# Performance work log

Hardware: AMD Instinct MI355X
Metric: run time of the kernel (lower is better)

Reference implementation:

```python
import jax, jax.numpy as jnp
import numpy as np

S = 2048        # q_len == context_length
HID = 4096      # hidden_size
NH = 32         # num_attention_heads
NKV = 8         # num_key_value_heads
HD = HID // NH  # head_dim = 128
THETA = 10000.0


def setup_inputs() -> dict:
    key = jax.random.key(0)
    ks = jax.random.split(key, 5)
    hidden_states = jax.random.normal(ks[0], (1, S, HID), dtype=jnp.float32)
    # 1x1 Conv2d weights == linear weights (out_ch, in_ch)
    wq = jax.random.normal(ks[1], (NH * HD, HID), dtype=jnp.float32) * 0.02
    wk = jax.random.normal(ks[2], (NKV * HD, HID), dtype=jnp.float32) * 0.02
    wv = jax.random.normal(ks[3], (NKV * HD, HID), dtype=jnp.float32) * 0.02
    wo = jax.random.normal(ks[4], (HID, NH * HD), dtype=jnp.float32) * 0.02
    # RoPE tables: rotate() only ever uses the first half_dim of cos/sin,
    # so build (1,1,S,half) directly (equivalent to cat(freqs,freqs) then slice).
    half = HD // 2
    inv_freq = 1.0 / (THETA ** (jnp.arange(0, HD, 2, dtype=jnp.float32) / HD))
    freqs = jnp.outer(jnp.arange(S, dtype=jnp.float32), inv_freq)  # (S, half)
    cos = jnp.cos(freqs)[None, None]  # (1,1,S,half)
    sin = jnp.sin(freqs)[None, None]
    # additive causal mask (1,1,S,S): 0 on/below diagonal, large negative above
    causal_mask = jnp.where(
        jnp.arange(S)[:, None] >= jnp.arange(S)[None, :], 0.0, -1e9
    ).astype(jnp.float32)[None, None]
    return dict(hidden_states=hidden_states, wq=wq, wk=wk, wv=wv, wo=wo,
                cos=cos, sin=sin, causal_mask=causal_mask)


def _rope(x, cos, sin):
    # x: (H, S, D); cos/sin: (1,1,S,D/2)
    half = x.shape[-1] // 2
    x1, x2 = x[..., :half], x[..., half:]
    c, s = cos[0, 0], sin[0, 0]  # (S, half), broadcasts over heads
    return jnp.concatenate([x1 * c - x2 * s, x2 * c + x1 * s], axis=-1)


def reference(hidden_states, wq, wk, wv, wo, cos, sin, causal_mask):
    x = hidden_states[0]               # (S, HID); bsz hard-coded to 1 in source
    seq = x.shape[0]
    # 1x1 conv projections == matmul; channel layout is head-major (h*HD + d)
    q = (x @ wq.T).reshape(seq, NH, HD).transpose(1, 0, 2)    # (NH, S, D)
    k = (x @ wk.T).reshape(seq, NKV, HD).transpose(1, 0, 2)   # (NKV, S, D)
    v = (x @ wv.T).reshape(seq, NKV, HD).transpose(1, 0, 2)   # (NKV, S, D)
    q = _rope(q, cos, sin)
    k = _rope(k, cos, sin)
    # repeat_kv: unsqueeze(1).repeat(n_rep).view -> head idx = rep*NKV + kv == tile
    n_rep = NH // NKV
    k = jnp.tile(k, (n_rep, 1, 1))     # (NH, S, D)
    v = jnp.tile(v, (n_rep, 1, 1))
    scale = 1.0 / np.sqrt(HD).astype(np.float32)
    scores = jnp.einsum('hqd,hkd->hqk', q, k) * scale + causal_mask[0, 0]
    attn = jax.nn.softmax(scores, axis=-1)                    # == ANE_softmax
    out = jnp.einsum('hqk,hkd->hqd', attn, v)                 # (NH, S, D)
    out = out.transpose(1, 0, 2).reshape(seq, NH * HD)        # (S, HID)
    return (out @ wo.T)[None]                                 # (1, S, HID)
```

## Files before the change

kernel.cpp:

```cpp
#include <hip/hip_runtime.h>
#include <hip/hip_bf16.h>

#define S_LEN 2048
#define HID   4096
#define NH    32
#define NKV   8
#define HD    128
#define QKV_N 6144
#define KDIM  4096

typedef __attribute__((ext_vector_type(8))) short short8;
typedef __attribute__((ext_vector_type(4))) float floatx4;
typedef unsigned short ushort;

__device__ __forceinline__ unsigned short f2bu(float f) {
  __hip_bfloat16 b = __float2bfloat16(f);
  return *reinterpret_cast<unsigned short*>(&b);
}
__device__ __forceinline__ void store_c(float* p, float v) { *p = v; }
__device__ __forceinline__ void store_c(__hip_bfloat16* p, float v) { *p = __float2bfloat16(v); }

__device__ __forceinline__ void async_copy16(const void* g, void* l) {
  __builtin_amdgcn_global_load_lds((const __attribute__((address_space(1))) void*)g,
                                   (__attribute__((address_space(3))) void*)l, 16, 0, 0);
}

struct bf16x4 { __hip_bfloat16 a, b, c, d; };
__global__ void cvt_f32_bf16(const float* __restrict__ src, __hip_bfloat16* __restrict__ dst, int n4) {
  int i = blockIdx.x * blockDim.x + threadIdx.x;
  if (i < n4) {
    float4 v = ((const float4*)src)[i];
    bf16x4 o = { __float2bfloat16(v.x), __float2bfloat16(v.y),
                 __float2bfloat16(v.z), __float2bfloat16(v.w) };
    ((bf16x4*)dst)[i] = o;
  }
}

template <typename CT>
__global__ __launch_bounds__(256, 2) void gemm_nt(const __hip_bfloat16* __restrict__ A,
                                                  const __hip_bfloat16* __restrict__ B,
                                                  CT* __restrict__ C, int M, int N, int K) {
  __shared__ __align__(16) ushort As[128 * 64];
  __shared__ __align__(16) ushort Bs[128 * 64];
  const int tid  = threadIdx.x;
  const int bm   = blockIdx.y * 128;
  const int bn   = blockIdx.x * 128;
  const int wave = tid >> 6;
  const int lane = tid & 63;
  const int ww   = (wave >> 1) * 64;
  const int wc   = (wave & 1) * 64;
  const int l15  = lane & 15;
  const int quad = lane >> 4;

  const ushort* Au = (const ushort*)A;
  const ushort* Bu = (const ushort*)B;

  const int rr  = lane >> 3;
  const int cc  = lane & 7;
  const int gch = cc ^ rr;
  const ushort* Ag = Au + (size_t)(bm + wave * 32 + rr) * K + gch * 8;
  const ushort* Bg = Bu + (size_t)(bn + wave * 32 + rr) * K + gch * 8;

  floatx4 acc[4][4] = {};

  for (int k0 = 0; k0 < K; k0 += 64) {
    __syncthreads();
#pragma unroll
    for (int e = 0; e < 4; ++e) {
      async_copy16(Ag + (size_t)(e * 8) * K + k0, &As[(wave * 32 + e * 8) * 64]);
      async_copy16(Bg + (size_t)(e * 8) * K + k0, &Bs[(wave * 32 + e * 8) * 64]);
    }
    __syncthreads();
#pragma unroll
    for (int kd = 0; kd < 2; ++kd) {
      short8 af[4], bf[4];
#pragma unroll
      for (int i = 0; i < 4; ++i) {
        af[i] = *(const short8*)&As[(ww + i * 16 + l15) * 64 + ((kd * 4 + quad) ^ (l15 & 7)) * 8];
        bf[i] = *(const short8*)&Bs[(wc + i * 16 + l15) * 64 + ((kd * 4 + quad) ^ (l15 & 7)) * 8];
      }
#pragma unroll
      for (int mi = 0; mi < 4; ++mi)
#pragma unroll
        for (int ni = 0; ni < 4; ++ni)
          acc[mi][ni] = __builtin_amdgcn_mfma_f32_16x16x32_bf16(af[mi], bf[ni], acc[mi][ni], 0, 0, 0);
    }
  }
#pragma unroll
  for (int mi = 0; mi < 4; ++mi)
#pragma unroll
    for (int ni = 0; ni < 4; ++ni)
#pragma unroll
      for (int r = 0; r < 4; ++r) {
        int row = bm + ww + mi * 16 + quad * 4 + r;
        int col = bn + wc + ni * 16 + l15;
        store_c(&C[(size_t)row * N + col], acc[mi][ni][r]);
      }
}

__global__ void rope_qk(const __hip_bfloat16* __restrict__ QKV,
                        const float* __restrict__ cosp, const float* __restrict__ sinp,
                        __hip_bfloat16* __restrict__ Qh, __hip_bfloat16* __restrict__ Kh) {
  int s = blockIdx.y;
  int col = blockIdx.x * 256 + threadIdx.x;
  if (col >= 5120) return;
  const size_t base = (size_t)s * QKV_N;
  float x = __bfloat162float(QKV[base + col]);
  int dd = col & 127;
  float val;
  if (dd < 64) {
    float xp = __bfloat162float(QKV[base + col + 64]);
    val = x * cosp[s * 64 + dd] - xp * sinp[s * 64 + dd];
  } else {
    int f = dd - 64;
    float xp = __bfloat162float(QKV[base + col - 64]);
    val = x * cosp[s * 64 + f] + xp * sinp[s * 64 + f];
  }
  if (col < HID) {
    int h = col >> 7;
    Qh[((size_t)h * S_LEN + s) * HD + dd] = __float2bfloat16(val);
  } else {
    int h = (col - HID) >> 7;
    Kh[((size_t)h * S_LEN + s) * HD + dd] = __float2bfloat16(val);
  }
}

__global__ void v_transpose(const __hip_bfloat16* __restrict__ QKV, __hip_bfloat16* __restrict__ Vt) {
  __shared__ ushort tile[64][130];
  int h = blockIdx.y;
  int s0 = blockIdx.x * 64;
  int t = threadIdx.x;
  const ushort* src = (const ushort*)QKV;
#pragma unroll
  for (int i = 0; i < 32; ++i) {
    int flat = i * 256 + t;
    int r = flat >> 7, c = flat & 127;
    tile[r][c] = src[(size_t)(s0 + r) * QKV_N + 5120 + h * 128 + c];
  }
  __syncthreads();
  ushort* dst = (ushort*)Vt;
#pragma unroll
  for (int i = 0; i < 8; ++i) {
    int g = i * 256 + t;
    int d = g >> 4, j4 = (g & 15) * 4;
    ushort4 o;
    o.x = tile[j4][d]; o.y = tile[j4 + 1][d]; o.z = tile[j4 + 2][d]; o.w = tile[j4 + 3][d];
    *(ushort4*)&dst[((size_t)h * HD + d) * S_LEN + s0 + j4] = o;
  }
}

__global__ __launch_bounds__(256, 2) void attn(const __hip_bfloat16* __restrict__ Qh,
                                               const __hip_bfloat16* __restrict__ Kh,
                                               const __hip_bfloat16* __restrict__ Vt,
                                               __hip_bfloat16* __restrict__ AO) {
  __shared__ __align__(16) ushort Ks[2][64][128];
  __shared__ __align__(16) ushort P[4][32][72];
  const int bi   = blockIdx.x;
  const int head = bi & 31;
  const int slot = (bi >> 5) & 7;
  const int qt   = (bi >= 256) ? (2 * slot) : (15 - 2 * slot);
  const int wave = threadIdx.x >> 6;
  const int lane = threadIdx.x & 63;
  const int l15 = lane & 15, quad = lane >> 4;
  const int q0 = qt * 128 + wave * 32;
  const int hk = head & 7;
  const ushort* Qu = (const ushort*)Qh + (size_t)head * S_LEN * HD;
  const ushort* Ku = (const ushort*)Kh + (size_t)hk * S_LEN * HD;
  const ushort* Vu = (const ushort*)Vt + (size_t)hk * HD * S_LEN;

  const int rr4  = lane >> 4;
  const int cc16 = lane & 15;

  short8 qf[2][4];
#pragma unroll
  for (int mt = 0; mt < 2; ++mt)
#pragma unroll
    for (int kd = 0; kd < 4; ++kd)
      qf[mt][kd] = *(const short8*)(Qu + (size_t)(q0 + mt * 16 + l15) * HD + kd * 32 + quad * 8);

  floatx4 o[2][8] = {};
  float mst[2][4], lsum[2][4];
#pragma unroll
  for (int mt = 0; mt < 2; ++mt)
#pragma unroll
    for (int r = 0; r < 4; ++r) { mst[mt][r] = -1e30f; lsum[mt][r] = 0.f; }

  const float scale = 0.08838834764831845f;
  const int nsteps = 2 * (qt + 1);
  const int jendw = q0 + 32;

  auto stage = [&](int b, int j0) {
#pragma unroll
    for (int e = 0; e < 4; ++e) {
      int rt = e * 4 + rr4;
      int gc = cc16 ^ rt;
      async_copy16(Ku + (size_t)(j0 + wave * 16 + rt) * HD + gc * 8,
                   &Ks[b][wave * 16 + e * 4][0]);
    }
  };
  stage(0, 0);

  for (int s = 0; s < nsteps; ++s) {
    const int j0 = s * 64;
    __syncthreads();
    if (s + 1 < nsteps) stage((s + 1) & 1, (s + 1) * 64);
    if (j0 >= jendw) continue;
    const int b = s & 1;

    short8 vf0[8];
#pragma unroll
    for (int t = 0; t < 8; ++t)
      vf0[t] = *(const short8*)(Vu + (size_t)(t * 16 + l15) * S_LEN + j0 + quad * 8);

    floatx4 sc[2][4];
#pragma unroll
    for (int mt = 0; mt < 2; ++mt)
#pragma unroll
      for (int nt = 0; nt < 4; ++nt) sc[mt][nt] = floatx4{0.f, 0.f, 0.f, 0.f};
#pragma unroll
    for (int nt = 0; nt < 4; ++nt) {
      short8 kf[4];
#pragma unroll
      for (int kd = 0; kd < 4; ++kd)
        kf[kd] = *(const short8*)&Ks[b][nt * 16 + l15][((kd * 4 + quad) ^ l15) * 8];
#pragma unroll
      for (int mt = 0; mt < 2; ++mt)
#pragma unroll
        for (int kd = 0; kd < 4; ++kd)
          sc[mt][nt] = __builtin_amdgcn_mfma_f32_16x16x32_bf16(qf[mt][kd], kf[kd], sc[mt][nt], 0, 0, 0);
    }

    const bool domask = (j0 + 64 > q0);
#pragma unroll
    for (int mt = 0; mt < 2; ++mt)
#pragma unroll
      for (int r = 0; r < 4; ++r) {
        const int row = q0 + mt * 16 + quad * 4 + r;
        float v[4];
#pragma unroll
        for (int nt = 0; nt < 4; ++nt) {
          float x = sc[mt][nt][r] * scale;
          if (domask && (j0 + nt * 16 + l15 > row)) x = -1e30f;
          v[nt] = x;
        }
        float vm = fmaxf(fmaxf(v[0], v[1]), fmaxf(v[2], v[3]));
        vm = fmaxf(vm, __shfl_xor(vm, 1));
        vm = fmaxf(vm, __shfl_xor(vm, 2));
        vm = fmaxf(vm, __shfl_xor(vm, 4));
        vm = fmaxf(vm, __shfl_xor(vm, 8));
        const float mnew = fmaxf(mst[mt][r], vm);
        const float alpha = __expf(mst[mt][r] - mnew);
        float ps = 0.f;
#pragma unroll
        for (int nt = 0; nt < 4; ++nt) {
          float p = __expf(v[nt] - mnew);
          ps += p;
          P[wave][mt * 16 + quad * 4 + r][nt * 16 + l15] = f2bu(p);
        }
        ps += __shfl_xor(ps, 1);
        ps += __shfl_xor(ps, 2);
        ps += __shfl_xor(ps, 4);
        ps += __shfl_xor(ps, 8);
        lsum[mt][r] = lsum[mt][r] * alpha + ps;
        mst[mt][r] = mnew;
#pragma unroll
        for (int t = 0; t < 8; ++t) o[mt][t][r] *= alpha;
      }

    short8 vf1[8];
#pragma unroll
    for (int t = 0; t < 8; ++t)
      vf1[t] = *(const short8*)(Vu + (size_t)(t * 16 + l15) * S_LEN + j0 + 32 + quad * 8);

    asm volatile("s_waitcnt lgkmcnt(0)" ::: "memory");
    short8 pf[2][2];
#pragma unroll
    for (int mt = 0; mt < 2; ++mt)
#pragma unroll
      for (int hh = 0; hh < 2; ++hh)
        pf[mt][hh] = *(const short8*)&P[wave][mt * 16 + l15][hh * 32 + quad * 8];
#pragma unroll
    for (int t = 0; t < 8; ++t)
#pragma unroll
      for (int mt = 0; mt < 2; ++mt) {
        o[mt][t] = __builtin_amdgcn_mfma_f32_16x16x32_bf16(pf[mt][0], vf0[t], o[mt][t], 0, 0, 0);
        o[mt][t] = __builtin_amdgcn_mfma_f32_16x16x32_bf16(pf[mt][1], vf1[t], o[mt][t], 0, 0, 0);
      }
  }

#pragma unroll
  for (int mt = 0; mt < 2; ++mt)
#pragma unroll
    for (int r = 0; r < 4; ++r) {
      const int row = q0 + mt * 16 + quad * 4 + r;
      const float inv = 1.0f / lsum[mt][r];
#pragma unroll
      for (int t = 0; t < 8; ++t)
        AO[(size_t)row * HID + head * HD + t * 16 + l15] = __float2bfloat16(o[mt][t][r] * inv);
    }
}

extern "C" void kernel_launch(void* const* d_in, const int* in_sizes, int n_in,
                              void* d_out, int out_size, void* d_ws, size_t ws_size,
                              hipStream_t stream) {
  const float* x    = (const float*)d_in[0];
  const float* wq   = (const float*)d_in[1];
  const float* wk   = (const float*)d_in[2];
  const float* wv   = (const float*)d_in[3];
  const float* wo   = (const float*)d_in[4];
  const float* cosp = (const float*)d_in[5];
  const float* sinp = (const float*)d_in[6];
  float* out = (float*)d_out;

  char* ws = (char*)d_ws;
  size_t off = 0;
  auto alloc = [&](size_t bytes) { char* p = ws + off; off += (bytes + 255) & ~255ull; return p; };
  __hip_bfloat16* Xb   = (__hip_bfloat16*)alloc((size_t)S_LEN * KDIM * 2);
  __hip_bfloat16* Wqkv = (__hip_bfloat16*)alloc((size_t)QKV_N * KDIM * 2);
  __hip_bfloat16* Wob  = (__hip_bfloat16*)alloc((size_t)HID * HID * 2);
  __hip_bfloat16* QKVb = (__hip_bfloat16*)alloc((size_t)S_LEN * QKV_N * 2);
  __hip_bfloat16* Qh   = (__hip_bfloat16*)alloc((size_t)NH * S_LEN * HD * 2);
  __hip_bfloat16* Kh   = (__hip_bfloat16*)alloc((size_t)NKV * S_LEN * HD * 2);
  __hip_bfloat16* Vt   = (__hip_bfloat16*)alloc((size_t)NKV * HD * S_LEN * 2);
  __hip_bfloat16* AO   = (__hip_bfloat16*)alloc((size_t)S_LEN * HID * 2);

  auto cvt = [&](const float* s, __hip_bfloat16* dpt, size_t n) {
    int n4 = (int)(n / 4);
    cvt_f32_bf16<<<dim3((n4 + 255) / 256), dim3(256), 0, stream>>>(s, dpt, n4);
  };
  cvt(x, Xb, (size_t)S_LEN * KDIM);
  cvt(wq, Wqkv, (size_t)HID * KDIM);
  cvt(wk, Wqkv + (size_t)HID * KDIM, (size_t)NKV * HD * KDIM);
  cvt(wv, Wqkv + (size_t)(HID + NKV * HD) * KDIM, (size_t)NKV * HD * KDIM);
  cvt(wo, Wob, (size_t)HID * HID);

  gemm_nt<__hip_bfloat16><<<dim3(QKV_N / 128, S_LEN / 128), dim3(256), 0, stream>>>(
      Xb, Wqkv, QKVb, S_LEN, QKV_N, KDIM);
  rope_qk<<<dim3(20, S_LEN), dim3(256), 0, stream>>>(QKVb, cosp, sinp, Qh, Kh);
  v_transpose<<<dim3(S_LEN / 64, NKV), dim3(256), 0, stream>>>(QKVb, Vt);
  attn<<<dim3(512), dim3(256), 0, stream>>>(Qh, Kh, Vt, AO);
  gemm_nt<float><<<dim3(HID / 128, S_LEN / 128), dim3(256), 0, stream>>>(
      AO, Wob, out, S_LEN, HID, KDIM);
}
```

Baseline: 587.7 us.

## Transpose QK^T MFMA so softmax rows live per lane; lazy rescale, prescaled Q

Swaps the MFMA operand order for S = QK^T so each lane holds one query row across 16 score values. Row max and sum then need only two cross-lane shuffles instead of four per row. Adds a lazy rescale that updates the running max and rescales O only when some row's max grows by more than 8, folds the softmax scale into Q during RoPE, and writes P to LDS as 4-element vectors. It also sets s_setprio around the MFMA blocks. The lazy threshold lets unnormalised exponentials grow up to e^8, which should stay safe in fp32 but costs a little bf16 precision in P.

```diff
diff --git a/kernel.cpp b/kernel.cpp
--- a/kernel.cpp
+++ b/kernel.cpp
@@ -118,7 +118,7 @@
   }
   if (col < HID) {
     int h = col >> 7;
-    Qh[((size_t)h * S_LEN + s) * HD + dd] = __float2bfloat16(val);
+    Qh[((size_t)h * S_LEN + s) * HD + dd] = __float2bfloat16(val * 0.08838834764831845f);
   } else {
     int h = (col - HID) >> 7;
     Kh[((size_t)h * S_LEN + s) * HD + dd] = __float2bfloat16(val);
@@ -179,13 +179,10 @@
       qf[mt][kd] = *(const short8*)(Qu + (size_t)(q0 + mt * 16 + l15) * HD + kd * 32 + quad * 8);
 
   floatx4 o[2][8] = {};
-  float mst[2][4], lsum[2][4];
-#pragma unroll
-  for (int mt = 0; mt < 2; ++mt)
-#pragma unroll
-    for (int r = 0; r < 4; ++r) { mst[mt][r] = -1e30f; lsum[mt][r] = 0.f; }
-
-  const float scale = 0.08838834764831845f;
+  float mst[2], lsum[2];
+  mst[0] = mst[1] = -1e30f;
+  lsum[0] = lsum[1] = 0.f;
+
   const int nsteps = 2 * (qt + 1);
   const int jendw = q0 + 32;
 
@@ -217,6 +214,7 @@
     for (int mt = 0; mt < 2; ++mt)
 #pragma unroll
       for (int nt = 0; nt < 4; ++nt) sc[mt][nt] = floatx4{0.f, 0.f, 0.f, 0.f};
+    __builtin_amdgcn_s_setprio(1);
 #pragma unroll
     for (int nt = 0; nt < 4; ++nt) {
       short8 kf[4];
@@ -227,45 +225,60 @@
       for (int mt = 0; mt < 2; ++mt)
 #pragma unroll
         for (int kd = 0; kd < 4; ++kd)
-          sc[mt][nt] = __builtin_amdgcn_mfma_f32_16x16x32_bf16(qf[mt][kd], kf[kd], sc[mt][nt], 0, 0, 0);
-    }
+          sc[mt][nt] = __builtin_amdgcn_mfma_f32_16x16x32_bf16(kf[kd], qf[mt][kd], sc[mt][nt], 0, 0, 0);
+    }
+    __builtin_amdgcn_s_setprio(0);
 
     const bool domask = (j0 + 64 > q0);
 #pragma unroll
-    for (int mt = 0; mt < 2; ++mt)
-#pragma unroll
-      for (int r = 0; r < 4; ++r) {
-        const int row = q0 + mt * 16 + quad * 4 + r;
-        float v[4];
-#pragma unroll
-        for (int nt = 0; nt < 4; ++nt) {
-          float x = sc[mt][nt][r] * scale;
-          if (domask && (j0 + nt * 16 + l15 > row)) x = -1e30f;
-          v[nt] = x;
+    for (int mt = 0; mt < 2; ++mt) {
+      const int qrow = q0 + mt * 16 + l15;
+      float pv[16];
+      float vm = -1e30f;
+#pragma unroll
+      for (int nt = 0; nt < 4; ++nt)
+#pragma unroll
+        for (int r = 0; r < 4; ++r) {
+          float x = sc[mt][nt][r];
+          if (domask && (j0 + nt * 16 + quad * 4 + r > qrow)) x = -1e30f;
+          pv[nt * 4 + r] = x;
+          vm = fmaxf(vm, x);
         }
-        float vm = fmaxf(fmaxf(v[0], v[1]), fmaxf(v[2], v[3]));
-        vm = fmaxf(vm, __shfl_xor(vm, 1));
-        vm = fmaxf(vm, __shfl_xor(vm, 2));
-        vm = fmaxf(vm, __shfl_xor(vm, 4));
-        vm = fmaxf(vm, __shfl_xor(vm, 8));
-        const float mnew = fmaxf(mst[mt][r], vm);
-        const float alpha = __expf(mst[mt][r] - mnew);
-        float ps = 0.f;
-#pragma unroll
-        for (int nt = 0; nt < 4; ++nt) {
-          float p = __expf(v[nt] - mnew);
-          ps += p;
-          P[wave][mt * 16 + quad * 4 + r][nt * 16 + l15] = f2bu(p);
-        }
-        ps += __shfl_xor(ps, 1);
-        ps += __shfl_xor(ps, 2);
-        ps += __shfl_xor(ps, 4);
-        ps += __shfl_xor(ps, 8);
-        lsum[mt][r] = lsum[mt][r] * alpha + ps;
-        mst[mt][r] = mnew;
-#pragma unroll
-        for (int t = 0; t < 8; ++t) o[mt][t][r] *= alpha;
-      }
+      vm = fmaxf(vm, __shfl_xor(vm, 16));
+      vm = fmaxf(vm, __shfl_xor(vm, 32));
+      if (__any(vm > mst[mt] + 8.0f)) {
+        const float mnew = fmaxf(mst[mt], vm);
+        const float alpha = __expf(mst[mt] - mnew);
+        mst[mt] = mnew;
+        lsum[mt] *= alpha;
+        float ar[4];
+#pragma unroll
+        for (int r = 0; r < 4; ++r)
+          ar[r] = __shfl(alpha, (lane & 48) | (quad * 4 + r));
+#pragma unroll
+        for (int t = 0; t < 8; ++t)
+#pragma unroll
+          for (int r = 0; r < 4; ++r) o[mt][t][r] *= ar[r];
+      }
+      float ps = 0.f;
+      ushort pk[16];
+#pragma unroll
+      for (int i = 0; i < 16; ++i) {
+        float p = __expf(pv[i] - mst[mt]);
+        ps += p;
+        pk[i] = f2bu(p);
+      }
+      ps += __shfl_xor(ps, 16);
+      ps += __shfl_xor(ps, 32);
+      lsum[mt] += ps;
+#pragma unroll
+      for (int nt = 0; nt < 4; ++nt) {
+        ushort4 w;
+        w.x = pk[nt * 4 + 0]; w.y = pk[nt * 4 + 1];
+        w.z = pk[nt * 4 + 2]; w.w = pk[nt * 4 + 3];
+        *(ushort4*)&P[wave][mt * 16 + l15][nt * 16 + quad * 4] = w;
+      }
+    }
 
     short8 vf1[8];
 #pragma unroll
@@ -279,6 +292,7 @@
 #pragma unroll
       for (int hh = 0; hh < 2; ++hh)
         pf[mt][hh] = *(const short8*)&P[wave][mt * 16 + l15][hh * 32 + quad * 8];
+    __builtin_amdgcn_s_setprio(1);
 #pragma unroll
     for (int t = 0; t < 8; ++t)
 #pragma unroll
@@ -286,18 +300,23 @@
         o[mt][t] = __builtin_amdgcn_mfma_f32_16x16x32_bf16(pf[mt][0], vf0[t], o[mt][t], 0, 0, 0);
         o[mt][t] = __builtin_amdgcn_mfma_f32_16x16x32_bf16(pf[mt][1], vf1[t], o[mt][t], 0, 0, 0);
       }
-  }
-
-#pragma unroll
-  for (int mt = 0; mt < 2; ++mt)
+    __builtin_amdgcn_s_setprio(0);
+  }
+
+#pragma unroll
+  for (int mt = 0; mt < 2; ++mt) {
+    float inv[4];
+#pragma unroll
+    for (int r = 0; r < 4; ++r)
+      inv[r] = 1.0f / __shfl(lsum[mt], (lane & 48) | (quad * 4 + r));
 #pragma unroll
     for (int r = 0; r < 4; ++r) {
       const int row = q0 + mt * 16 + quad * 4 + r;
-      const float inv = 1.0f / lsum[mt][r];
 #pragma unroll
       for (int t = 0; t < 8; ++t)
-        AO[(size_t)row * HID + head * HD + t * 16 + l15] = __float2bfloat16(o[mt][t][r] * inv);
-    }
+        AO[(size_t)row * HID + head * HD + t * 16 + l15] = __float2bfloat16(o[mt][t][r] * inv[r]);
+    }
+  }
 }
 
 extern "C" void kernel_launch(void* const* d_in, const int* in_sizes, int n_in,
```

Result: faster. 551.7 us (-6.1%).
